# Optimization experiments

Hardware: AMD Instinct MI355X
Metric: run time of the kernel (lower is better)

The kernel has to match this reference:

```python
import jax, jax.numpy as jnp
import numpy as np

N, T, D, H = 256, 512, 256, 256


def setup_inputs() -> dict:
    key = jax.random.key(0)
    ks = jax.random.split(key, 9)
    scale_x = float(np.sqrt(6.0 / (D + H)))  # xavier_uniform range approx
    scale_h = float(np.sqrt(6.0 / (H + H)))
    def wx(k):
        return jax.random.uniform(k, (D, H), jnp.float32, -scale_x, scale_x)
    def wh(k):
        return jax.random.uniform(k, (H, H), jnp.float32, -scale_h, scale_h)
    inp = {
        'x': jax.random.normal(ks[0], (N, T, D), jnp.float32),
        'w_ii': wx(ks[1]), 'w_hi': wh(ks[2]),
        'w_if': wx(ks[3]), 'w_hf': wh(ks[4]),
        'w_ig': wx(ks[5]), 'w_hg': wh(ks[6]),
        'w_io': wx(ks[7]), 'w_ho': wh(ks[8]),
        # init_hidden() zeros all 1-D params
        'b_ii': jnp.zeros((H,), jnp.float32), 'b_hi': jnp.zeros((H,), jnp.float32),
        'b_if': jnp.zeros((H,), jnp.float32), 'b_hf': jnp.zeros((H,), jnp.float32),
        'b_ig': jnp.zeros((H,), jnp.float32), 'b_hg': jnp.zeros((H,), jnp.float32),
        'b_io': jnp.zeros((H,), jnp.float32), 'b_ho': jnp.zeros((H,), jnp.float32),
    }
    return inp


def reference(x, w_ii, w_hi, w_if, w_hf, w_ig, w_hg, w_io, w_ho,
              b_ii, b_hi, b_if, b_hf, b_ig, b_hg, b_io, b_ho):
    # Fuse the 4 input projections and 4 hidden projections into 2 GEMMs
    # (mathematically identical to the 8 separate matmuls).
    Wx = jnp.concatenate([w_ii, w_if, w_ig, w_io], axis=1)  # (D, 4H)
    Wh = jnp.concatenate([w_hi, w_hf, w_hg, w_ho], axis=1)  # (H, 4H)
    b = jnp.concatenate([b_ii + b_hi, b_if + b_hf, b_ig + b_hg, b_io + b_ho])  # (4H,)
    n, t, _ = x.shape
    h = x.shape[2]  # noqa (not used)
    # Precompute input projections for all timesteps: (T, N, 4H)
    xW = jnp.einsum('ntd,dg->tng', x, Wx)
    h0 = jnp.zeros((n, w_hi.shape[0]), x.dtype)
    c0 = jnp.zeros_like(h0)

    def step(carry, xw_t):
        h_t, c_t = carry
        gates = xw_t + h_t @ Wh + b  # (N, 4H)
        i_t, f_t, g_t, o_t = jnp.split(gates, 4, axis=1)
        i_t = jax.nn.sigmoid(i_t)
        f_t = jax.nn.sigmoid(f_t)
        g_t = jnp.tanh(g_t)
        o_t = jax.nn.sigmoid(o_t)
        c_t = f_t * c_t + i_t * g_t
        h_t = o_t * jnp.tanh(c_t)
        return (h_t, c_t), None

    (h_T, c_T), _ = jax.lax.scan(step, (h0, c0), xW)
    return (h_T, c_T)
```

## Files before the change

### kernel.cpp

```cpp
#include <hip/hip_runtime.h>
#include <cstdint>

typedef float  f32x4  __attribute__((ext_vector_type(4)));
typedef __bf16 bf16x8 __attribute__((ext_vector_type(8)));
typedef int    i32x4  __attribute__((ext_vector_type(4)));
typedef unsigned short u16;
typedef u16 u16x4 __attribute__((ext_vector_type(4)));

#define TT 512

__device__ __forceinline__ u16 f2bf(float f) {
  unsigned u = __builtin_bit_cast(unsigned, f);
  unsigned r = u + 0x7fffu + ((u >> 16) & 1u);
  return (u16)(r >> 16);
}
__device__ __forceinline__ float bflo(unsigned d) { return __builtin_bit_cast(float, d << 16); }
__device__ __forceinline__ float bfhi(unsigned d) { return __builtin_bit_cast(float, d & 0xffff0000u); }
__device__ __forceinline__ float rcpf(float x) { return __builtin_amdgcn_rcpf(x); }
__device__ __forceinline__ float fsig(float x) { return rcpf(1.f + __expf(-x)); }
__device__ __forceinline__ float ftanh(float x) { return 1.f - 2.f * rcpf(1.f + __expf(2.f * x)); }
__device__ __forceinline__ void gload_lds16(const u16* g, u16* l) {
  __builtin_amdgcn_global_load_lds((const __attribute__((address_space(1))) void*)(g),
                                   (__attribute__((address_space(3))) void*)(l), 16, 0, 0);
}

__global__ __launch_bounds__(512, 2) void lstm_fused(
    const float* __restrict__ X,
    const float* __restrict__ wii, const float* __restrict__ whi,
    const float* __restrict__ wif, const float* __restrict__ whf,
    const float* __restrict__ wig, const float* __restrict__ whg,
    const float* __restrict__ wio, const float* __restrict__ who,
    const float* __restrict__ bii, const float* __restrict__ bhi,
    const float* __restrict__ bif, const float* __restrict__ bhf,
    const float* __restrict__ big_, const float* __restrict__ bhg,
    const float* __restrict__ bio, const float* __restrict__ bho,
    u16* __restrict__ Wxb, signed char* __restrict__ Whq,
    float* __restrict__ wscale, float* __restrict__ bsum,
    u16* __restrict__ xWp, int* __restrict__ rprog, float* __restrict__ out) {
  __shared__ u16 As[128 * 256];
  __shared__ u16 Bh[2][128 * 128];
  __shared__ __align__(16) signed char hb[2][576];
  int p = blockIdx.x;
  int tid = threadIdx.x;

  if (p >= 128) {
    int k = p - 128;

    {
      int cl = tid >> 6, dl = tid & 63;
      int C = k * 8 + cl;
      int G = C >> 8, h = C & 255;
      const float* wxp[4] = {wii, wif, wig, wio};
      const float* whp[4] = {whi, whf, whg, who};
      const float* sx = wxp[G];
#pragma unroll
      for (int i = 0; i < 4; ++i) {
        int d = i * 64 + dl;
        Wxb[(size_t)C * 256 + d] = f2bf(sx[(size_t)d * 256 + h]);
      }
      const float* sh = whp[G];
      float wv[4];
      float am = 0.f;
#pragma unroll
      for (int i = 0; i < 4; ++i) {
        int d = i * 64 + dl;
        wv[i] = sh[(size_t)d * 256 + h];
        am = fmaxf(am, fabsf(wv[i]));
      }
#pragma unroll
      for (int off = 32; off > 0; off >>= 1)
        am = fmaxf(am, __shfl_xor(am, off, 64));
      float scale = (am > 0.f) ? am * (1.f / 127.f) : 1.f;
      if (dl == 0) wscale[C] = scale * (1.f / 127.f);
#pragma unroll
      for (int i = 0; i < 4; ++i) {
        float qf = rintf(wv[i] / scale);
        qf = fminf(127.f, fmaxf(-127.f, qf));
        Whq[(size_t)C * 256 + i * 64 + dl] = (signed char)(int)qf;
      }
      if (k == 0 && tid < 256) {
        const float* bx[4] = {bii, bif, big_, bio};
        const float* bh4[4] = {bhi, bhf, bhg, bho};
        for (int Gg = 0; Gg < 4; ++Gg) bsum[Gg * 256 + tid] = bx[Gg][tid] + bh4[Gg][tid];
      }
      __syncthreads();
      if (tid == 0)
        __hip_atomic_fetch_add(&rprog[8], 1, __ATOMIC_RELEASE, __HIP_MEMORY_SCOPE_AGENT);
      if (tid == 0) {
        while (__hip_atomic_load(&rprog[8], __ATOMIC_RELAXED, __HIP_MEMORY_SCOPE_AGENT) < 128)
          __builtin_amdgcn_s_sleep(8);
        (void)__hip_atomic_load(&rprog[8], __ATOMIC_ACQUIRE, __HIP_MEMORY_SCOPE_AGENT);
      }
      __syncthreads();
    }

    const u16* Bt = Wxb;
    int l = tid & 63, w8 = tid >> 6;
    int wm = w8 >> 2, wn = w8 & 3;
    int c = l & 15, q = l >> 4;
    int sw = (c & 7) << 4;
    int rowbase[4];
#pragma unroll
    for (int mt = 0; mt < 4; ++mt) rowbase[mt] = (wm * 64 + mt * 16 + c) * 512;

#define STAGE_BH(BN, HALF, BUF)                                                 \
    {                                                                           \
      _Pragma("unroll")                                                         \
      for (int s2 = 0; s2 < 4; ++s2) {                                          \
        int i = s2 * 512 + tid;                                                 \
        int cl2 = i >> 4, wk = i & 15;                                          \
        gload_lds16(Bt + (size_t)((BN) * 128 + cl2) * 256 + (HALF) * 128 +      \
                        ((wk * 8) ^ ((cl2 & 7) << 3)),                          \
                    &Bh[BUF][0] + i * 8);                                       \
      }                                                                         \
    }

    for (int j = 0; j < 8; ++j) {
      int bm = j * 128 + k;
      __syncthreads();
      STAGE_BH(0, 0, 0)
#pragma unroll 4
      for (int jj = 0; jj < 16; ++jj) {
        int row_l = jj * 8 + w8;
        int d = l * 4;
        int r = bm * 128 + row_l;
        int t = r >> 8, n = r & 255;
        const float4 v = *(const float4*)(X + ((size_t)n * 512 + t) * 256 + d);
        u16x4 pk;
        pk[0] = f2bf(v.x); pk[1] = f2bf(v.y); pk[2] = f2bf(v.z); pk[3] = f2bf(v.w);
        int ba = (row_l * 512 + l * 8) ^ ((row_l & 7) << 4);
        *(u16x4*)((char*)As + ba) = pk;
      }
      __syncthreads();

      f32x4 acc[4][2];
#pragma unroll
      for (int i = 0; i < 4; ++i)
#pragma unroll
        for (int jn = 0; jn < 2; ++jn) acc[i][jn] = (f32x4){0.f, 0.f, 0.f, 0.f};

      for (int s = 0; s < 16; ++s) {
        int bn = s >> 1, half = s & 1, buf = s & 1;
        if (s < 15) {
          int sn = s + 1;
          STAGE_BH(sn >> 1, sn & 1, buf ^ 1)
        }
        const u16* bp = &Bh[buf][0];
#pragma unroll
        for (int kk = 0; kk < 4; ++kk) {
          int ko = half * 4 + kk;
          bf16x8 af[4], bfr[2];
          int koff  = (ko * 64 + q * 16) ^ sw;
          int koffb = (kk * 64 + q * 16) ^ sw;
#pragma unroll
          for (int mt = 0; mt < 4; ++mt)
            af[mt] = *(const bf16x8*)((const char*)As + rowbase[mt] + koff);
#pragma unroll
          for (int nt = 0; nt < 2; ++nt)
            bfr[nt] = *(const bf16x8*)((const char*)bp + (size_t)(wn * 32 + nt * 16 + c) * 256 + koffb);
#pragma unroll
          for (int mt = 0; mt < 4; ++mt)
#pragma unroll
            for (int nt = 0; nt < 2; ++nt)
              acc[mt][nt] = __builtin_amdgcn_mfma_f32_16x16x32_bf16(af[mt], bfr[nt], acc[mt][nt], 0, 0, 0);
        }
        if (half == 1) {
#pragma unroll
          for (int mt = 0; mt < 4; ++mt) {
            int tm = bm * 8 + wm * 4 + mt;
#pragma unroll
            for (int nt = 0; nt < 2; ++nt) {
              int tn = bn * 8 + wn * 2 + nt;
              float bv = bsum[tn * 16 + c];
              u16x4 pk;
#pragma unroll
              for (int r = 0; r < 4; ++r) pk[r] = f2bf(acc[mt][nt][r] + bv);
              *reinterpret_cast<u16x4*>(xWp + ((size_t)(tm * 64 + tn) * 256 + l * 4)) = pk;
              acc[mt][nt] = (f32x4){0.f, 0.f, 0.f, 0.f};
            }
          }
        }
        __syncthreads();
      }
      if (tid == 0)
        __hip_atomic_fetch_add(&rprog[j], 1, __ATOMIC_RELEASE, __HIP_MEMORY_SCOPE_AGENT);
    }
#undef STAGE_BH
    return;
  }

  int xcd = p & 7, q8 = (p >> 3) & 7, tsel = p >> 6;
  int G = xcd * 2 + tsel;
  int wid = tid >> 6, l = tid & 63;
  int c = l & 15, q = (l >> 4) & 3;
  int tt = q >> 1, rsel = q & 1;

  for (int i = tid; i < 288; i += 512) ((int*)hb)[i] = 0;

  if (tid == 0) {
    while (__hip_atomic_load(&rprog[8], __ATOMIC_RELAXED, __HIP_MEMORY_SCOPE_AGENT) < 128)
      __builtin_amdgcn_s_sleep(8);
    (void)__hip_atomic_load(&rprog[8], __ATOMIC_ACQUIRE, __HIP_MEMORY_SCOPE_AGENT);
  }
  __syncthreads();

  i32x4 bw[4][2][4];
#pragma unroll
  for (int g = 0; g < 4; ++g)
#pragma unroll
    for (int ttl = 0; ttl < 2; ++ttl) {
      int col = g * 256 + wid * 32 + ttl * 16 + c;
#pragma unroll
      for (int ks = 0; ks < 4; ++ks)
        bw[g][ttl][ks] = *reinterpret_cast<const i32x4*>(Whq + (size_t)col * 256 + ks * 64 + q * 16);
    }
  float sc8[4];
#pragma unroll
  for (int g = 0; g < 4; ++g) sc8[g] = wscale[g * 256 + wid * 32 + tt * 16 + c];

  const char* xbase = (const char*)xWp + (size_t)G * 32768;
  int xoff[4];
#pragma unroll
  for (int g = 0; g < 4; ++g) {
    int tn = g * 16 + wid * 2 + tt;
    xoff[g] = tn * 512 + (((q8 >> 1) * 16 + c) * 8) + (q8 & 1) * 4;
  }

  if (tid == 0) {
    while (__hip_atomic_load(&rprog[0], __ATOMIC_RELAXED, __HIP_MEMORY_SCOPE_AGENT) < 128)
      __builtin_amdgcn_s_sleep(8);
    (void)__hip_atomic_load(&rprog[0], __ATOMIC_ACQUIRE, __HIP_MEMORY_SCOPE_AGENT);
  }
  __syncthreads();

  unsigned xw0[4], xw1[4];
#pragma unroll
  for (int g = 0; g < 4; ++g) xw0[g] = *(const unsigned*)(xbase + xoff[g]);
  xbase += 524288;

  i32x4 zacc = (i32x4){0, 0, 0, 0};
  float cs = 0.f, hh = 0.f;
  __syncthreads();

#define STEP(CUR, XW_CUR, XW_NXT)                                               \
  {                                                                             \
    _Pragma("unroll")                                                           \
    for (int g = 0; g < 4; ++g) XW_NXT[g] = *(const unsigned*)(xbase + xoff[g]);\
    const signed char* hr = hb[CUR ^ 1];                                        \
    i32x4 acc[4][2];                                                            \
    {                                                                           \
      i32x4 a0 = *(const i32x4*)(hr + (c & 1) * 288 + q * 16);                  \
      _Pragma("unroll")                                                         \
      for (int g = 0; g < 4; ++g) {                                             \
        __asm__("v_mfma_i32_16x16x64_i8 %0, %1, %2, %3"                         \
                : "=&v"(acc[g][0]) : "v"(a0), "a"(bw[g][0][0]), "v"(zacc));     \
        __asm__("v_mfma_i32_16x16x64_i8 %0, %1, %2, %3"                         \
                : "=&v"(acc[g][1]) : "v"(a0), "a"(bw[g][1][0]), "v"(zacc));     \
      }                                                                         \
    }                                                                           \
    _Pragma("unroll")                                                           \
    for (int ks = 1; ks < 4; ++ks) {                                            \
      i32x4 a = *(const i32x4*)(hr + (c & 1) * 288 + ks * 64 + q * 16);         \
      _Pragma("unroll")                                                         \
      for (int g = 0; g < 4; ++g) {                                             \
        __asm__("v_mfma_i32_16x16x64_i8 %0, %1, %2, %0"                         \
                : "+v"(acc[g][0]) : "v"(a), "a"(bw[g][0][ks]));                 \
        __asm__("v_mfma_i32_16x16x64_i8 %0, %1, %2, %0"                         \
                : "+v"(acc[g][1]) : "v"(a), "a"(bw[g][1][ks]));                 \
      }                                                                         \
    }                                                                           \
    __asm__ volatile("s_nop 7\n\ts_nop 7\n\ts_nop 7");   \
    float a4[4];                                                                \
    _Pragma("unroll")                                                           \
    for (int g = 0; g < 4; ++g) {                                               \
      int e = tt ? (rsel ? acc[g][1][1] : acc[g][1][0])                         \
                 : (rsel ? acc[g][0][1] : acc[g][0][0]);                        \
      unsigned d = XW_CUR[g];                                                   \
      float xv = rsel ? bfhi(d) : bflo(d);                                      \
      a4[g] = (float)e * sc8[g] + xv;                                           \
    }                                                                           \
    float gi = fsig(a4[0]);                                                     \
    float gf = fsig(a4[1]);                                                     \
    float gg = ftanh(a4[2]);                                                    \
    float go = fsig(a4[3]);                                                     \
    cs = gf * cs + gi * gg;                                                     \
    hh = go * ftanh(cs);                                                        \
    int hq = (int)rintf(hh * 127.f);                                            \
    hb[CUR][rsel * 288 + wid * 32 + tt * 16 + c] = (signed char)hq;             \
    xbase += 524288;                                                            \
    __builtin_amdgcn_s_waitcnt(0xC07F);   \
    __builtin_amdgcn_s_barrier();                                               \
  }

  for (int t = 0; t < TT; t += 2) {
    STEP(0, xw0, xw1)
    if (((t + 2) & 63) == 0 && (t + 2) < TT) {
      int j = (t + 2) >> 6;
      if (tid == 0) {
        while (__hip_atomic_load(&rprog[j], __ATOMIC_RELAXED, __HIP_MEMORY_SCOPE_AGENT) < 128)
          __builtin_amdgcn_s_sleep(8);
        (void)__hip_atomic_load(&rprog[j], __ATOMIC_ACQUIRE, __HIP_MEMORY_SCOPE_AGENT);
      }
      __syncthreads();
    }
    STEP(1, xw1, xw0)
  }
#undef STEP

  {
    int n = G * 16 + q8 * 2 + rsel;
    int hu = wid * 32 + tt * 16 + c;
    out[(size_t)n * 256 + hu] = hh;
    out[65536 + (size_t)n * 256 + hu] = cs;
  }
}

extern "C" void kernel_launch(void* const* d_in, const int* in_sizes, int n_in,
                              void* d_out, int out_size, void* d_ws, size_t ws_size,
                              hipStream_t stream) {
  const float* x   = (const float*)d_in[0];
  const float* wii = (const float*)d_in[1];
  const float* whi = (const float*)d_in[2];
  const float* wif = (const float*)d_in[3];
  const float* whf = (const float*)d_in[4];
  const float* wig = (const float*)d_in[5];
  const float* whg = (const float*)d_in[6];
  const float* wio = (const float*)d_in[7];
  const float* who = (const float*)d_in[8];
  const float* bii = (const float*)d_in[9];
  const float* bhi = (const float*)d_in[10];
  const float* bif = (const float*)d_in[11];
  const float* bhf = (const float*)d_in[12];
  const float* big_ = (const float*)d_in[13];
  const float* bhg = (const float*)d_in[14];
  const float* bio = (const float*)d_in[15];
  const float* bho = (const float*)d_in[16];

  char* ws = (char*)d_ws;
  int*   rprog  = (int*)(ws);
  u16*   Wxb    = (u16*)(ws + 67108864);
  signed char* Whq = (signed char*)(ws + 67633152);
  float* wscale = (float*)(ws + 67895296);
  float* bsum   = (float*)(ws + 67899392);
  u16*   xWp    = (u16*)(ws + 67903488);
  float* out = (float*)d_out;

  hipMemsetAsync(rprog, 0, 64, stream);
  lstm_fused<<<256, 512, 0, stream>>>(x,
                                      wii, whi, wif, whf, wig, whg, wio, who,
                                      bii, bhi, bif, bhf, big_, bhg, bio, bho,
                                      Wxb, Whq, wscale, bsum, xWp, rprog, out);
}
```

Baseline: 630.8 us.

## Load Wx B-fragments directly from global in MFMA-ready layout, drop LDS staging

Stores the bf16 input-projection weight in a k-chunked [K/8][4H][8] layout so each lane can fetch its MFMA B fragment with one 16-byte global load. The double-buffered LDS staging of B and the per-substep __syncthreads inside the projection GEMM are removed. The aim is fewer barriers and less LDS traffic in the producer blocks that compute xW. The cost is B fragments served from L2/global with no LDS reuse, which adds load latency. The As shared array is also enlarged to 164 rows, presumably to change occupancy or padding.

```diff
diff --git a/kernel.cpp b/kernel.cpp
--- a/kernel.cpp
+++ b/kernel.cpp
@@ -19,10 +19,6 @@
 __device__ __forceinline__ float rcpf(float x) { return __builtin_amdgcn_rcpf(x); }
 __device__ __forceinline__ float fsig(float x) { return rcpf(1.f + __expf(-x)); }
 __device__ __forceinline__ float ftanh(float x) { return 1.f - 2.f * rcpf(1.f + __expf(2.f * x)); }
-__device__ __forceinline__ void gload_lds16(const u16* g, u16* l) {
-  __builtin_amdgcn_global_load_lds((const __attribute__((address_space(1))) void*)(g),
-                                   (__attribute__((address_space(3))) void*)(l), 16, 0, 0);
-}
 
 __global__ __launch_bounds__(512, 2) void lstm_fused(
     const float* __restrict__ X,
@@ -34,11 +30,10 @@
     const float* __restrict__ bif, const float* __restrict__ bhf,
     const float* __restrict__ big_, const float* __restrict__ bhg,
     const float* __restrict__ bio, const float* __restrict__ bho,
-    u16* __restrict__ Wxb, signed char* __restrict__ Whq,
+    u16* __restrict__ WxbKC, signed char* __restrict__ Whq,
     float* __restrict__ wscale, float* __restrict__ bsum,
     u16* __restrict__ xWp, int* __restrict__ rprog, float* __restrict__ out) {
-  __shared__ u16 As[128 * 256];
-  __shared__ u16 Bh[2][128 * 128];
+  __shared__ u16 As[164 * 256];
   __shared__ __align__(16) signed char hb[2][576];
   int p = blockIdx.x;
   int tid = threadIdx.x;
@@ -56,7 +51,8 @@
 #pragma unroll
       for (int i = 0; i < 4; ++i) {
         int d = i * 64 + dl;
-        Wxb[(size_t)C * 256 + d] = f2bf(sx[(size_t)d * 256 + h]);
+        WxbKC[((size_t)(i * 8 + (dl >> 3)) * 1024 + C) * 8 + (dl & 7)] =
+            f2bf(sx[(size_t)d * 256 + h]);
       }
       const float* sh = whp[G];
       float wv[4];
@@ -94,7 +90,6 @@
       __syncthreads();
     }
 
-    const u16* Bt = Wxb;
     int l = tid & 63, w8 = tid >> 6;
     int wm = w8 >> 2, wn = w8 & 3;
     int c = l & 15, q = l >> 4;
@@ -103,22 +98,9 @@
 #pragma unroll
     for (int mt = 0; mt < 4; ++mt) rowbase[mt] = (wm * 64 + mt * 16 + c) * 512;
 
-#define STAGE_BH(BN, HALF, BUF)                                                 \
-    {                                                                           \
-      _Pragma("unroll")                                                         \
-      for (int s2 = 0; s2 < 4; ++s2) {                                          \
-        int i = s2 * 512 + tid;                                                 \
-        int cl2 = i >> 4, wk = i & 15;                                          \
-        gload_lds16(Bt + (size_t)((BN) * 128 + cl2) * 256 + (HALF) * 128 +      \
-                        ((wk * 8) ^ ((cl2 & 7) << 3)),                          \
-                    &Bh[BUF][0] + i * 8);                                       \
-      }                                                                         \
-    }
-
     for (int j = 0; j < 8; ++j) {
       int bm = j * 128 + k;
       __syncthreads();
-      STAGE_BH(0, 0, 0)
 #pragma unroll 4
       for (int jj = 0; jj < 16; ++jj) {
         int row_l = jj * 8 + w8;
@@ -139,53 +121,43 @@
 #pragma unroll
         for (int jn = 0; jn < 2; ++jn) acc[i][jn] = (f32x4){0.f, 0.f, 0.f, 0.f};
 
-      for (int s = 0; s < 16; ++s) {
-        int bn = s >> 1, half = s & 1, buf = s & 1;
-        if (s < 15) {
-          int sn = s + 1;
-          STAGE_BH(sn >> 1, sn & 1, buf ^ 1)
-        }
-        const u16* bp = &Bh[buf][0];
-#pragma unroll
-        for (int kk = 0; kk < 4; ++kk) {
-          int ko = half * 4 + kk;
+      for (int bn = 0; bn < 8; ++bn) {
+        const u16* bsrc0 = WxbKC + (size_t)q * 8192 + (bn * 128 + wn * 32 + c) * 8;
+#pragma unroll
+        for (int ko = 0; ko < 8; ++ko) {
           bf16x8 af[4], bfr[2];
-          int koff  = (ko * 64 + q * 16) ^ sw;
-          int koffb = (kk * 64 + q * 16) ^ sw;
+          int koff = (ko * 64 + q * 16) ^ sw;
 #pragma unroll
           for (int mt = 0; mt < 4; ++mt)
             af[mt] = *(const bf16x8*)((const char*)As + rowbase[mt] + koff);
-#pragma unroll
-          for (int nt = 0; nt < 2; ++nt)
-            bfr[nt] = *(const bf16x8*)((const char*)bp + (size_t)(wn * 32 + nt * 16 + c) * 256 + koffb);
+          const u16* bsrc = bsrc0 + (size_t)ko * 32768;
+          bfr[0] = *(const bf16x8*)(bsrc);
+          bfr[1] = *(const bf16x8*)(bsrc + 128);
 #pragma unroll
           for (int mt = 0; mt < 4; ++mt)
 #pragma unroll
             for (int nt = 0; nt < 2; ++nt)
               acc[mt][nt] = __builtin_amdgcn_mfma_f32_16x16x32_bf16(af[mt], bfr[nt], acc[mt][nt], 0, 0, 0);
         }
-        if (half == 1) {
-#pragma unroll
-          for (int mt = 0; mt < 4; ++mt) {
-            int tm = bm * 8 + wm * 4 + mt;
-#pragma unroll
-            for (int nt = 0; nt < 2; ++nt) {
-              int tn = bn * 8 + wn * 2 + nt;
-              float bv = bsum[tn * 16 + c];
-              u16x4 pk;
-#pragma unroll
-              for (int r = 0; r < 4; ++r) pk[r] = f2bf(acc[mt][nt][r] + bv);
-              *reinterpret_cast<u16x4*>(xWp + ((size_t)(tm * 64 + tn) * 256 + l * 4)) = pk;
-              acc[mt][nt] = (f32x4){0.f, 0.f, 0.f, 0.f};
-            }
+#pragma unroll
+        for (int mt = 0; mt < 4; ++mt) {
+          int tm = bm * 8 + wm * 4 + mt;
+#pragma unroll
+          for (int nt = 0; nt < 2; ++nt) {
+            int tn = bn * 8 + wn * 2 + nt;
+            float bv = bsum[tn * 16 + c];
+            u16x4 pk;
+#pragma unroll
+            for (int r = 0; r < 4; ++r) pk[r] = f2bf(acc[mt][nt][r] + bv);
+            *reinterpret_cast<u16x4*>(xWp + ((size_t)(tm * 64 + tn) * 256 + l * 4)) = pk;
+            acc[mt][nt] = (f32x4){0.f, 0.f, 0.f, 0.f};
           }
         }
-        __syncthreads();
-      }
+      }
+      __syncthreads();
       if (tid == 0)
         __hip_atomic_fetch_add(&rprog[j], 1, __ATOMIC_RELEASE, __HIP_MEMORY_SCOPE_AGENT);
     }
-#undef STAGE_BH
     return;
   }
 
@@ -338,7 +310,7 @@
 
   char* ws = (char*)d_ws;
   int*   rprog  = (int*)(ws);
-  u16*   Wxb    = (u16*)(ws + 67108864);
+  u16*   WxbKC  = (u16*)(ws + 67108864);
   signed char* Whq = (signed char*)(ws + 67633152);
   float* wscale = (float*)(ws + 67895296);
   float* bsum   = (float*)(ws + 67899392);
@@ -349,5 +321,5 @@
   lstm_fused<<<256, 512, 0, stream>>>(x,
                                       wii, whi, wif, whf, wig, whg, wio, who,
                                       bii, bhi, bif, bhf, big_, bhg, bio, bho,
-                                      Wxb, Whq, wscale, bsum, xWp, rprog, out);
+                                      WxbKC, Whq, wscale, bsum, xWp, rprog, out);
 }
```

Measured after the change: 640.5 us. About the same (+1.5%).
